# Kernel optimization log

Hardware: AMD Instinct MI355X
Metric: run time of the kernel (lower is better)

The kernel has to match this reference:

```python
import jax, jax.numpy as jnp
import numpy as np

B, C, NP, NT, D = 512, 3, 49, 76, 768
EPS = 0.1        # Sinkhorn entropic regularization
THRESH = 0.01    # convergence threshold on mean |r - r0|
MAX_ITER = 100


def _normalize(x, axis=-1):
    n = jnp.linalg.norm(x, axis=axis, keepdims=True)
    return x / jnp.maximum(n, 1e-12)


def _sinkhorn(K, u, v):
    # K: [B, n, m], u: [B, n], v: [B, m]. Faithful to the torch loop with
    # early exit: do-while via lax.while_loop (err check after each update).
    def cond(state):
        _, _, err, i = state
        return (i < MAX_ITER) & (err >= THRESH)

    def body(state):
        r, c, _, i = state
        r_new = u / jnp.einsum('bnm,bm->bn', K, c)
        c_new = v / jnp.einsum('bnm,bn->bm', K, r_new)
        err = jnp.mean(jnp.abs(r_new - r))
        return (r_new, c_new, err, i + 1)

    r0 = jnp.ones_like(u)
    c0 = jnp.ones_like(v)
    r, c, _, _ = jax.lax.while_loop(
        cond, body, (r0, c0, jnp.asarray(jnp.inf, K.dtype), 0))
    return r[..., :, None] * c[..., None, :] * K  # transport plan T


def _cross_entropy(logits):
    # labels = arange(B) (diagonal targets)
    logp = jax.nn.log_softmax(logits, axis=-1)
    return -jnp.mean(jnp.diagonal(logp))


def setup_inputs() -> dict:
    key = jax.random.key(0)
    k1, k2, k3, k4 = jax.random.split(key, 4)
    return {
        'image_features': jax.random.normal(k1, (B, C, D), jnp.float32),
        'text_features': jax.random.normal(k2, (B, C, D), jnp.float32),
        'logit_scale': jnp.full((1,), 100.0, jnp.float32),
        'local_image_features': jax.random.normal(k3, (B, C, NP, D), jnp.float32),
        'local_text_features': jax.random.normal(k4, (B, C, NT, D), jnp.float32),
    }


def reference(image_features, text_features, logit_scale,
              local_image_features, local_text_features):
    scale = logit_scale.reshape(())
    li = _normalize(local_image_features)          # [B, C, 49, D]
    lt = _normalize(local_text_features)           # [B, C, 76, D]
    # per-channel token similarity: [B, C, 49, 76]
    sim = jnp.einsum('bcnd,bcmd->bcnm', li, lt)
    # Sinkhorn is under no_grad in the original -> stop_gradient on K and T.
    K = jax.lax.stop_gradient(jnp.exp(-(1.0 - sim) / EPS))
    u = jnp.full((B, NP), 1.0 / NP, sim.dtype)
    v = jnp.full((B, NT), 1.0 / NT, sim.dtype)
    ot_loss = jnp.asarray(0.0, sim.dtype)
    for ch in range(C):  # per-channel Sinkhorn (independent early stopping)
        T = jax.lax.stop_gradient(_sinkhorn(K[:, ch], u, v))
        ot_loss = ot_loss + jnp.sum(T * sim[:, ch])
    # logits averaged over the 3 channels (sum over c folded into einsum)
    logits_per_image = scale * jnp.einsum(
        'bcd,ncd->bn', image_features, text_features) / C
    logits_per_text = logits_per_image.T
    total_loss = (_cross_entropy(logits_per_image)
                  + _cross_entropy(logits_per_text)) / 2 + ot_loss
    return total_loss
```

## Files before the change

### kernel.cpp

```cpp
#include <hip/hip_runtime.h>

#define NB 512
#define NC 3
#define NP_ 49
#define NT_ 76
#define DD 768

typedef __attribute__((ext_vector_type(8))) short bf16x8;
typedef __attribute__((ext_vector_type(4))) float f32x4;

__device__ inline unsigned short f2bf(float x) {
    unsigned int u = __float_as_uint(x);
    u += 0x7FFFu + ((u >> 16) & 1u);
    return (unsigned short)(u >> 16);
}
__device__ inline float bf_lo(unsigned int w) { return __uint_as_float(w << 16); }
__device__ inline float bf_hi(unsigned int w) { return __uint_as_float(w & 0xFFFF0000u); }

__global__ __launch_bounds__(256) void sink_kernel(const float* __restrict__ lif,
                                                   const float* __restrict__ ltf,
                                                   float* __restrict__ out) {
    const int tid = threadIdx.x;
    const int bc  = blockIdx.x;
    const float* ga = lif + (size_t)bc * (NP_ * DD);
    const float* gb = ltf + (size_t)bc * (NT_ * DD);

    __shared__ __attribute__((aligned(16))) unsigned short a_buf[64 * 72];
    __shared__ __attribute__((aligned(16))) unsigned short b_buf[80 * 72];
    __shared__ float Kmat[NP_ * 77];
    __shared__ float s_inv[144];
    __shared__ float r_vec[64];
    __shared__ float c_vec[80];
    __shared__ float s_err[4];
    __shared__ float s_red[4];

    for (int idx = tid; idx < 15 * 72; idx += 256) a_buf[49 * 72 + idx] = 0;
    for (int idx = tid; idx < 4 * 72;  idx += 256) b_buf[76 * 72 + idx] = 0;

    const int wave = tid >> 6;
    const int lane = tid & 63;
    const int lr = lane & 15;
    const int lk = lane >> 4;

    f32x4 acc[4][5];
    const f32x4 zero4 = {0.f, 0.f, 0.f, 0.f};
#pragma unroll
    for (int tn = 0; tn < 4; ++tn)
#pragma unroll
        for (int j = 0; j < 5; ++j) acc[tn][j] = zero4;

    float na = 0.f, nb = 0.f;

    for (int cc = 0; cc < 12; ++cc) {
        const int k0 = cc * 64;
        for (int idx = tid; idx < NP_ * 16; idx += 256) {
            int row = idx >> 4, q = idx & 15;
            const float4 v = *(const float4*)(ga + row * DD + k0 + q * 4);
            unsigned int w0 = (unsigned int)f2bf(v.x) | ((unsigned int)f2bf(v.y) << 16);
            unsigned int w1 = (unsigned int)f2bf(v.z) | ((unsigned int)f2bf(v.w) << 16);
            *(uint2*)(a_buf + row * 72 + q * 4) = make_uint2(w0, w1);
        }
        for (int idx = tid; idx < NT_ * 16; idx += 256) {
            int row = idx >> 4, q = idx & 15;
            const float4 v = *(const float4*)(gb + row * DD + k0 + q * 4);
            unsigned int w0 = (unsigned int)f2bf(v.x) | ((unsigned int)f2bf(v.y) << 16);
            unsigned int w1 = (unsigned int)f2bf(v.z) | ((unsigned int)f2bf(v.w) << 16);
            *(uint2*)(b_buf + row * 72 + q * 4) = make_uint2(w0, w1);
        }
        __syncthreads();
        if (wave == 0) {
#pragma unroll
            for (int ks = 0; ks < 2; ++ks) {
                bf16x8 bv[5];
#pragma unroll
                for (int j = 0; j < 5; ++j)
                    bv[j] = *(const bf16x8*)(b_buf + (j * 16 + lr) * 72 + ks * 32 + lk * 8);
#pragma unroll
                for (int tn = 0; tn < 4; ++tn) {
                    bf16x8 av = *(const bf16x8*)(a_buf + (tn * 16 + lr) * 72 + ks * 32 + lk * 8);
#pragma unroll
                    for (int j = 0; j < 5; ++j)
                        acc[tn][j] = __builtin_amdgcn_mfma_f32_16x16x32_bf16(av, bv[j], acc[tn][j], 0, 0, 0);
                }
            }
        } else if (wave == 1) {
            if (lane < NP_) {
                const unsigned int* ap = (const unsigned int*)(a_buf + lane * 72);
#pragma unroll
                for (int k = 0; k < 32; ++k) {
                    unsigned int w = ap[k];
                    float x = bf_lo(w), y = bf_hi(w);
                    na += x * x + y * y;
                }
            }
        } else {
            int j = tid - 128;
            if (j < NT_) {
                const unsigned int* bp = (const unsigned int*)(b_buf + j * 72);
#pragma unroll
                for (int k = 0; k < 32; ++k) {
                    unsigned int w = bp[k];
                    float x = bf_lo(w), y = bf_hi(w);
                    nb += x * x + y * y;
                }
            }
        }
        __syncthreads();
    }

    if (wave == 1 && lane < NP_) s_inv[lane] = 1.0f / fmaxf(sqrtf(na), 1e-12f);
    if (tid >= 128 && (tid - 128) < NT_) s_inv[64 + (tid - 128)] = 1.0f / fmaxf(sqrtf(nb), 1e-12f);
    __syncthreads();

    if (wave == 0) {
#pragma unroll
        for (int tn = 0; tn < 4; ++tn)
#pragma unroll
            for (int j = 0; j < 5; ++j)
#pragma unroll
                for (int rg = 0; rg < 4; ++rg) {
                    int n = tn * 16 + lk * 4 + rg;
                    int m = j * 16 + lr;
                    if (n < NP_ && m < NT_) {
                        float simv = acc[tn][j][rg] * s_inv[n] * s_inv[64 + m];
                        Kmat[n * 77 + m] = __expf((simv - 1.0f) * 10.0f);
                    }
                }
    }
    if (tid < NT_) c_vec[tid] = 1.0f;
    __syncthreads();

    const int n1 = tid >> 2, seg1 = tid & 3;
    const int n1c = (n1 < NP_) ? n1 : 0;
    float Kv1[19];
#pragma unroll
    for (int i = 0; i < 19; ++i)
        Kv1[i] = (tid < 196) ? Kmat[n1c * 77 + seg1 * 19 + i] : 0.0f;

    const int m2 = tid >> 1, seg2 = tid & 1;
    const int n2base = seg2 * 25;
    float Kv2[25];
#pragma unroll
    for (int i = 0; i < 25; ++i) {
        int nn = n2base + i;
        int nc = (nn < NP_) ? nn : 0;
        Kv2[i] = (tid < 152 && nn < NP_) ? Kmat[nc * 77 + m2] : 0.0f;
    }

    float r_old = 1.0f;
    float err;
    int iter = 0;
    do {
        float y = 0.f;
#pragma unroll
        for (int i = 0; i < 19; ++i) y += Kv1[i] * c_vec[seg1 * 19 + i];
        y += __shfl_xor(y, 1);
        y += __shfl_xor(y, 2);
        float rn = (1.0f / 49.0f) / y;
        float de = 0.f;
        if (tid < 196) {
            de = fabsf(rn - r_old);
            r_old = rn;
            if (seg1 == 0) r_vec[n1] = rn;
        }
        float e = de;
#pragma unroll
        for (int o = 1; o < 64; o <<= 1) e += __shfl_xor(e, o);
        if (lane == 0) s_err[wave] = e;
        __syncthreads();
        err = (s_err[0] + s_err[1] + s_err[2] + s_err[3]) * (1.0f / (4.0f * 49.0f));

        float z = 0.f;
#pragma unroll
        for (int i = 0; i < 25; ++i) {
            int nn = n2base + i;
            z += Kv2[i] * r_vec[(nn < NP_) ? nn : 0];
        }
        z += __shfl_xor(z, 1);
        if (tid < 152 && seg2 == 0) c_vec[m2] = (1.0f / 76.0f) / z;
        ++iter;
        __syncthreads();
    } while (iter < 100 && err >= 1e-3f);

    float part = 0.f;
    for (int e0 = tid; e0 < NP_ * NT_; e0 += 256) {
        int n = e0 / NT_;
        int m = e0 - n * NT_;
        float kv = Kmat[n * 77 + m];
        part += r_vec[n] * c_vec[m] * kv * (__logf(kv) * 0.1f + 1.0f);
    }
#pragma unroll
    for (int o = 1; o < 64; o <<= 1) part += __shfl_xor(part, o);
    if (lane == 0) s_red[wave] = part;
    __syncthreads();
    if (tid == 0) atomicAdd(out, s_red[0] + s_red[1] + s_red[2] + s_red[3]);
}

__global__ __launch_bounds__(256) void gemm_logits(const float* __restrict__ A,
                                                   const float* __restrict__ Bm,
                                                   float* __restrict__ L) {
    __shared__ __attribute__((aligned(16))) float At[64 * 36];
    __shared__ __attribute__((aligned(16))) float Bt[64 * 36];
    const int tid = threadIdx.x;
    const int i0 = blockIdx.x * 64, j0 = blockIdx.y * 64, kbase = blockIdx.z * 576;
    const int ty = tid >> 4, tx = tid & 15;
    float accv[4][4] = {};
    for (int kc = 0; kc < 18; ++kc) {
        int kb = kbase + kc * 32;
#pragma unroll
        for (int t = 0; t < 2; ++t) {
            int idx = tid + t * 256;
            int row = idx >> 3, q = idx & 7;
            *(float4*)(At + row * 36 + q * 4) =
                *(const float4*)(A + (size_t)(i0 + row) * 2304 + kb + q * 4);
            *(float4*)(Bt + row * 36 + q * 4) =
                *(const float4*)(Bm + (size_t)(j0 + row) * 2304 + kb + q * 4);
        }
        __syncthreads();
#pragma unroll 8
        for (int k = 0; k < 32; ++k) {
            float ra[4], rb[4];
#pragma unroll
            for (int a = 0; a < 4; ++a) ra[a] = At[(ty + 16 * a) * 36 + k];
#pragma unroll
            for (int b = 0; b < 4; ++b) rb[b] = Bt[(tx + 16 * b) * 36 + k];
#pragma unroll
            for (int a = 0; a < 4; ++a)
#pragma unroll
                for (int b = 0; b < 4; ++b) accv[a][b] += ra[a] * rb[b];
        }
        __syncthreads();
    }
#pragma unroll
    for (int a = 0; a < 4; ++a)
#pragma unroll
        for (int b = 0; b < 4; ++b)
            atomicAdd(L + (size_t)(i0 + ty + 16 * a) * 512 + (j0 + tx + 16 * b), accv[a][b]);
}

__device__ inline float blk_max(float v, float* sred, int wave, int lane) {
#pragma unroll
    for (int o = 1; o < 64; o <<= 1) v = fmaxf(v, __shfl_xor(v, o));
    if (lane == 0) sred[wave] = v;
    __syncthreads();
    v = fmaxf(fmaxf(sred[0], sred[1]), fmaxf(sred[2], sred[3]));
    __syncthreads();
    return v;
}
__device__ inline float blk_sum(float v, float* sred, int wave, int lane) {
#pragma unroll
    for (int o = 1; o < 64; o <<= 1) v += __shfl_xor(v, o);
    if (lane == 0) sred[wave] = v;
    __syncthreads();
    v = sred[0] + sred[1] + sred[2] + sred[3];
    __syncthreads();
    return v;
}

__global__ __launch_bounds__(256) void ce_kernel(const float* __restrict__ L,
                                                 const float* __restrict__ lsc,
                                                 float* __restrict__ out) {
    __shared__ float sred[4];
    const int i = blockIdx.x, tid = threadIdx.x;
    const int wave = tid >> 6, lane = tid & 63;
    const float s = lsc[0] * (1.0f / 3.0f);

    float xr0 = L[(size_t)i * 512 + tid] * s;
    float xr1 = L[(size_t)i * 512 + tid + 256] * s;
    float xc0 = L[(size_t)tid * 512 + i] * s;
    float xc1 = L[(size_t)(tid + 256) * 512 + i] * s;

    float mr = blk_max(fmaxf(xr0, xr1), sred, wave, lane);
    float sr = blk_sum(__expf(xr0 - mr) + __expf(xr1 - mr), sred, wave, lane);
    float lse_r = mr + __logf(sr);

    float mc = blk_max(fmaxf(xc0, xc1), sred, wave, lane);
    float sc = blk_sum(__expf(xc0 - mc) + __expf(xc1 - mc), sred, wave, lane);
    float lse_c = mc + __logf(sc);

    if (tid == 0) {
        float dii = L[(size_t)i * 512 + i] * s;
        atomicAdd(out, (lse_r + lse_c - 2.0f * dii) * (1.0f / 1024.0f));
    }
}

extern "C" void kernel_launch(void* const* d_in, const int* in_sizes, int n_in,
                              void* d_out, int out_size, void* d_ws, size_t ws_size,
                              hipStream_t stream) {
    const float* img = (const float*)d_in[0];
    const float* txt = (const float*)d_in[1];
    const float* lsc = (const float*)d_in[2];
    const float* lif = (const float*)d_in[3];
    const float* ltf = (const float*)d_in[4];
    float* out = (float*)d_out;
    float* Lws = (float*)d_ws;

    hipMemsetAsync(out, 0, sizeof(float), stream);
    hipMemsetAsync(Lws, 0, 512 * 512 * sizeof(float), stream);

    hipLaunchKernelGGL(gemm_logits, dim3(8, 8, 4), dim3(256), 0, stream, img, txt, Lws);
    hipLaunchKernelGGL(sink_kernel, dim3(NB * NC), dim3(256), 0, stream, lif, ltf, out);
    hipLaunchKernelGGL(ce_kernel, dim3(512), dim3(256), 0, stream, Lws, lsc, out);
}
```

Measured before the change: 763.0 us.

## Run Sinkhorn per channel in a single wave with direct global MFMA loads

Rewrites the Sinkhorn kernel to use one 64-lane wave per (batch, channel) block. The wave loads fp32 features straight from global memory into MFMA fragments, fusing the bf16 conversion and the norm accumulation, so the LDS staging and the block barriers go away. The Sinkhorn iterations keep K rows and columns in registers and reduce with wave shuffles, with no __syncthreads. This carries heavy register pressure (Kr, Kc and Kc2 arrays) and loses inter-wave parallelism within a block. Separately, the logits GEMM's split-K factor is doubled from 4 to 8.

```diff
diff --git a/kernel.cpp b/kernel.cpp
--- a/kernel.cpp
+++ b/kernel.cpp
@@ -14,33 +14,52 @@
     u += 0x7FFFu + ((u >> 16) & 1u);
     return (unsigned short)(u >> 16);
 }
-__device__ inline float bf_lo(unsigned int w) { return __uint_as_float(w << 16); }
-__device__ inline float bf_hi(unsigned int w) { return __uint_as_float(w & 0xFFFF0000u); }
-
-__global__ __launch_bounds__(256) void sink_kernel(const float* __restrict__ lif,
-                                                   const float* __restrict__ ltf,
-                                                   float* __restrict__ out) {
-    const int tid = threadIdx.x;
-    const int bc  = blockIdx.x;
+__device__ inline float bfval(unsigned short s) {
+    return __uint_as_float((unsigned int)s << 16);
+}
+__device__ inline float f4get(const float4& v, int e) {
+    return e == 0 ? v.x : e == 1 ? v.y : e == 2 ? v.z : v.w;
+}
+
+__device__ inline bf16x8 pack8(const float4& lo, const float4& hi, float& nrm) {
+    bf16x8 r;
+    unsigned short s; float x;
+    s = f2bf(lo.x); x = bfval(s); nrm += x * x; r[0] = (short)s;
+    s = f2bf(lo.y); x = bfval(s); nrm += x * x; r[1] = (short)s;
+    s = f2bf(lo.z); x = bfval(s); nrm += x * x; r[2] = (short)s;
+    s = f2bf(lo.w); x = bfval(s); nrm += x * x; r[3] = (short)s;
+    s = f2bf(hi.x); x = bfval(s); nrm += x * x; r[4] = (short)s;
+    s = f2bf(hi.y); x = bfval(s); nrm += x * x; r[5] = (short)s;
+    s = f2bf(hi.z); x = bfval(s); nrm += x * x; r[6] = (short)s;
+    s = f2bf(hi.w); x = bfval(s); nrm += x * x; r[7] = (short)s;
+    return r;
+}
+
+__global__ __launch_bounds__(64, 2) void sink_kernel(const float* __restrict__ lif,
+                                                     const float* __restrict__ ltf,
+                                                     float* __restrict__ out) {
+    const int lane = threadIdx.x;
+    const int bc   = blockIdx.x;
+    const int lr = lane & 15, lk = lane >> 4;
     const float* ga = lif + (size_t)bc * (NP_ * DD);
     const float* gb = ltf + (size_t)bc * (NT_ * DD);
 
-    __shared__ __attribute__((aligned(16))) unsigned short a_buf[64 * 72];
-    __shared__ __attribute__((aligned(16))) unsigned short b_buf[80 * 72];
     __shared__ float Kmat[NP_ * 77];
-    __shared__ float s_inv[144];
-    __shared__ float r_vec[64];
-    __shared__ float c_vec[80];
-    __shared__ float s_err[4];
-    __shared__ float s_red[4];
-
-    for (int idx = tid; idx < 15 * 72; idx += 256) a_buf[49 * 72 + idx] = 0;
-    for (int idx = tid; idx < 4 * 72;  idx += 256) b_buf[76 * 72 + idx] = 0;
-
-    const int wave = tid >> 6;
-    const int lane = tid & 63;
-    const int lr = lane & 15;
-    const int lk = lane >> 4;
+    __shared__ __attribute__((aligned(16))) float c_vec[80];
+    __shared__ __attribute__((aligned(16))) float r_vec[64];
+
+    const float* pa[4];
+#pragma unroll
+    for (int tn = 0; tn < 4; ++tn) {
+        int row = tn * 16 + lr; if (row > NP_ - 1) row = NP_ - 1;
+        pa[tn] = ga + row * DD + lk * 8;
+    }
+    const float* pb[5];
+#pragma unroll
+    for (int j = 0; j < 5; ++j) {
+        int row = j * 16 + lr; if (row > NT_ - 1) row = NT_ - 1;
+        pb[j] = gb + row * DD + lk * 8;
+    }
 
     f32x4 acc[4][5];
     const f32x4 zero4 = {0.f, 0.f, 0.f, 0.f};
@@ -48,152 +67,151 @@
     for (int tn = 0; tn < 4; ++tn)
 #pragma unroll
         for (int j = 0; j < 5; ++j) acc[tn][j] = zero4;
-
-    float na = 0.f, nb = 0.f;
-
-    for (int cc = 0; cc < 12; ++cc) {
-        const int k0 = cc * 64;
-        for (int idx = tid; idx < NP_ * 16; idx += 256) {
-            int row = idx >> 4, q = idx & 15;
-            const float4 v = *(const float4*)(ga + row * DD + k0 + q * 4);
-            unsigned int w0 = (unsigned int)f2bf(v.x) | ((unsigned int)f2bf(v.y) << 16);
-            unsigned int w1 = (unsigned int)f2bf(v.z) | ((unsigned int)f2bf(v.w) << 16);
-            *(uint2*)(a_buf + row * 72 + q * 4) = make_uint2(w0, w1);
-        }
-        for (int idx = tid; idx < NT_ * 16; idx += 256) {
-            int row = idx >> 4, q = idx & 15;
-            const float4 v = *(const float4*)(gb + row * DD + k0 + q * 4);
-            unsigned int w0 = (unsigned int)f2bf(v.x) | ((unsigned int)f2bf(v.y) << 16);
-            unsigned int w1 = (unsigned int)f2bf(v.z) | ((unsigned int)f2bf(v.w) << 16);
-            *(uint2*)(b_buf + row * 72 + q * 4) = make_uint2(w0, w1);
-        }
-        __syncthreads();
-        if (wave == 0) {
-#pragma unroll
-            for (int ks = 0; ks < 2; ++ks) {
-                bf16x8 bv[5];
-#pragma unroll
-                for (int j = 0; j < 5; ++j)
-                    bv[j] = *(const bf16x8*)(b_buf + (j * 16 + lr) * 72 + ks * 32 + lk * 8);
-#pragma unroll
-                for (int tn = 0; tn < 4; ++tn) {
-                    bf16x8 av = *(const bf16x8*)(a_buf + (tn * 16 + lr) * 72 + ks * 32 + lk * 8);
-#pragma unroll
-                    for (int j = 0; j < 5; ++j)
-                        acc[tn][j] = __builtin_amdgcn_mfma_f32_16x16x32_bf16(av, bv[j], acc[tn][j], 0, 0, 0);
-                }
-            }
-        } else if (wave == 1) {
-            if (lane < NP_) {
-                const unsigned int* ap = (const unsigned int*)(a_buf + lane * 72);
-#pragma unroll
-                for (int k = 0; k < 32; ++k) {
-                    unsigned int w = ap[k];
-                    float x = bf_lo(w), y = bf_hi(w);
-                    na += x * x + y * y;
-                }
-            }
-        } else {
-            int j = tid - 128;
-            if (j < NT_) {
-                const unsigned int* bp = (const unsigned int*)(b_buf + j * 72);
-#pragma unroll
-                for (int k = 0; k < 32; ++k) {
-                    unsigned int w = bp[k];
-                    float x = bf_lo(w), y = bf_hi(w);
-                    nb += x * x + y * y;
-                }
-            }
-        }
-        __syncthreads();
-    }
-
-    if (wave == 1 && lane < NP_) s_inv[lane] = 1.0f / fmaxf(sqrtf(na), 1e-12f);
-    if (tid >= 128 && (tid - 128) < NT_) s_inv[64 + (tid - 128)] = 1.0f / fmaxf(sqrtf(nb), 1e-12f);
-    __syncthreads();
-
-    if (wave == 0) {
+    float na[4] = {0.f, 0.f, 0.f, 0.f};
+    float nb[5] = {0.f, 0.f, 0.f, 0.f, 0.f};
+
+#pragma unroll 1
+    for (int cc = 0; cc < 24; ++cc) {
+        const int off = cc * 32;
+        float4 a0[4], a1[4], b0[5], b1[5];
+#pragma unroll
+        for (int tn = 0; tn < 4; ++tn) {
+            a0[tn] = *(const float4*)(pa[tn] + off);
+            a1[tn] = *(const float4*)(pa[tn] + off + 4);
+        }
+#pragma unroll
+        for (int j = 0; j < 5; ++j) {
+            b0[j] = *(const float4*)(pb[j] + off);
+            b1[j] = *(const float4*)(pb[j] + off + 4);
+        }
+        bf16x8 af[4], bfr[5];
+#pragma unroll
+        for (int tn = 0; tn < 4; ++tn) af[tn] = pack8(a0[tn], a1[tn], na[tn]);
+#pragma unroll
+        for (int j = 0; j < 5; ++j)  bfr[j] = pack8(b0[j], b1[j], nb[j]);
 #pragma unroll
         for (int tn = 0; tn < 4; ++tn)
 #pragma unroll
             for (int j = 0; j < 5; ++j)
-#pragma unroll
-                for (int rg = 0; rg < 4; ++rg) {
-                    int n = tn * 16 + lk * 4 + rg;
-                    int m = j * 16 + lr;
-                    if (n < NP_ && m < NT_) {
-                        float simv = acc[tn][j][rg] * s_inv[n] * s_inv[64 + m];
+                acc[tn][j] = __builtin_amdgcn_mfma_f32_16x16x32_bf16(af[tn], bfr[j], acc[tn][j], 0, 0, 0);
+    }
+
+#pragma unroll
+    for (int tn = 0; tn < 4; ++tn) {
+        float v = na[tn];
+        v += __shfl_xor(v, 16);
+        v += __shfl_xor(v, 32);
+        na[tn] = 1.0f / fmaxf(sqrtf(v), 1e-12f);
+    }
+#pragma unroll
+    for (int j = 0; j < 5; ++j) {
+        float v = nb[j];
+        v += __shfl_xor(v, 16);
+        v += __shfl_xor(v, 32);
+        nb[j] = 1.0f / fmaxf(sqrtf(v), 1e-12f);
+    }
+
+#pragma unroll
+    for (int tn = 0; tn < 4; ++tn)
+#pragma unroll
+        for (int rg = 0; rg < 4; ++rg) {
+            const int n = tn * 16 + lk * 4 + rg;
+            const float ia = __shfl(na[tn], lk * 4 + rg);
+            if (n < NP_) {
+#pragma unroll
+                for (int j = 0; j < 5; ++j) {
+                    const int m = j * 16 + lr;
+                    if (m < NT_) {
+                        const float simv = acc[tn][j][rg] * ia * nb[j];
                         Kmat[n * 77 + m] = __expf((simv - 1.0f) * 10.0f);
                     }
                 }
-    }
-    if (tid < NT_) c_vec[tid] = 1.0f;
-    __syncthreads();
-
-    const int n1 = tid >> 2, seg1 = tid & 3;
-    const int n1c = (n1 < NP_) ? n1 : 0;
-    float Kv1[19];
-#pragma unroll
-    for (int i = 0; i < 19; ++i)
-        Kv1[i] = (tid < 196) ? Kmat[n1c * 77 + seg1 * 19 + i] : 0.0f;
-
-    const int m2 = tid >> 1, seg2 = tid & 1;
-    const int n2base = seg2 * 25;
-    float Kv2[25];
-#pragma unroll
-    for (int i = 0; i < 25; ++i) {
-        int nn = n2base + i;
-        int nc = (nn < NP_) ? nn : 0;
-        Kv2[i] = (tid < 152 && nn < NP_) ? Kmat[nc * 77 + m2] : 0.0f;
+            }
+        }
+
+    c_vec[lane] = 1.0f;
+    if (lane < 16) c_vec[64 + lane] = 1.0f;
+
+    const int nrow = (lane < NP_) ? lane : 0;
+    float Kr[NT_];
+#pragma unroll
+    for (int m = 0; m < NT_; ++m)
+        Kr[m] = (lane < NP_) ? Kmat[nrow * 77 + m] : 0.0f;
+
+    const int col2 = (lane < 12) ? (64 + lane) : (NT_ - 1);
+    float Kc[NP_], Kc2[NP_];
+#pragma unroll
+    for (int n = 0; n < NP_; ++n) {
+        Kc[n]  = Kmat[n * 77 + lane];
+        Kc2[n] = Kmat[n * 77 + col2];
     }
 
     float r_old = 1.0f;
     float err;
     int iter = 0;
     do {
-        float y = 0.f;
-#pragma unroll
-        for (int i = 0; i < 19; ++i) y += Kv1[i] * c_vec[seg1 * 19 + i];
-        y += __shfl_xor(y, 1);
-        y += __shfl_xor(y, 2);
-        float rn = (1.0f / 49.0f) / y;
-        float de = 0.f;
-        if (tid < 196) {
-            de = fabsf(rn - r_old);
-            r_old = rn;
-            if (seg1 == 0) r_vec[n1] = rn;
-        }
+        float y0 = 0.f, y1 = 0.f, y2 = 0.f, y3 = 0.f;
+#pragma unroll
+        for (int q = 0; q < 19; ++q) {
+            const float4 cq = *(const float4*)(c_vec + q * 4);
+#pragma unroll
+            for (int e = 0; e < 4; ++e) {
+                const int i = 4 * q + e;
+                const float cv = f4get(cq, e);
+                if (i < 19)      y0 += Kr[i] * cv;
+                else if (i < 38) y1 += Kr[i] * cv;
+                else if (i < 57) y2 += Kr[i] * cv;
+                else             y3 += Kr[i] * cv;
+            }
+        }
+        const float y  = (y0 + y1) + (y2 + y3);
+        const float rn = (1.0f / 49.0f) / y;
+        const float de = (lane < NP_) ? fabsf(rn - r_old) : 0.0f;
+        r_old = rn;
+        r_vec[lane] = rn;
+
         float e = de;
-#pragma unroll
-        for (int o = 1; o < 64; o <<= 1) e += __shfl_xor(e, o);
-        if (lane == 0) s_err[wave] = e;
-        __syncthreads();
-        err = (s_err[0] + s_err[1] + s_err[2] + s_err[3]) * (1.0f / (4.0f * 49.0f));
-
-        float z = 0.f;
-#pragma unroll
-        for (int i = 0; i < 25; ++i) {
-            int nn = n2base + i;
-            z += Kv2[i] * r_vec[(nn < NP_) ? nn : 0];
-        }
-        z += __shfl_xor(z, 1);
-        if (tid < 152 && seg2 == 0) c_vec[m2] = (1.0f / 76.0f) / z;
+        e += __shfl_xor(e, 1);
+        e += __shfl_xor(e, 2);
+        e += __shfl_xor(e, 4);
+        e += __shfl_xor(e, 8);
+        const float g0 = __shfl(e, 0),  g1 = __shfl(e, 16);
+        const float g2 = __shfl(e, 32), g3 = __shfl(e, 48);
+        err = (((g0 + g1) + g2) + g3) * (1.0f / 49.0f);
+
+        float z0 = 0.f, z1 = 0.f, w0 = 0.f, w1 = 0.f;
+#pragma unroll
+        for (int q = 0; q < 13; ++q) {
+            const float4 rq = *(const float4*)(r_vec + q * 4);
+#pragma unroll
+            for (int e2 = 0; e2 < 4; ++e2) {
+                const int n = 4 * q + e2;
+                const float rv = f4get(rq, e2);
+                if (n < 25)      { z0 += Kc[n] * rv; w0 += Kc2[n] * rv; }
+                else if (n < 49) { z1 += Kc[n] * rv; w1 += Kc2[n] * rv; }
+            }
+        }
+        c_vec[lane] = (1.0f / 76.0f) / (z0 + z1);
+        if (lane < 12) c_vec[64 + lane] = (1.0f / 76.0f) / (w0 + w1);
         ++iter;
-        __syncthreads();
     } while (iter < 100 && err >= 1e-3f);
 
     float part = 0.f;
-    for (int e0 = tid; e0 < NP_ * NT_; e0 += 256) {
-        int n = e0 / NT_;
-        int m = e0 - n * NT_;
-        float kv = Kmat[n * 77 + m];
-        part += r_vec[n] * c_vec[m] * kv * (__logf(kv) * 0.1f + 1.0f);
+    if (lane < NP_) {
+        const float rr = r_old;
+#pragma unroll
+        for (int q = 0; q < 19; ++q) {
+            const float4 cq = *(const float4*)(c_vec + q * 4);
+#pragma unroll
+            for (int e2 = 0; e2 < 4; ++e2) {
+                const float kv = Kr[4 * q + e2];
+                part += rr * f4get(cq, e2) * kv * (__logf(kv) * 0.1f + 1.0f);
+            }
+        }
     }
 #pragma unroll
     for (int o = 1; o < 64; o <<= 1) part += __shfl_xor(part, o);
-    if (lane == 0) s_red[wave] = part;
-    __syncthreads();
-    if (tid == 0) atomicAdd(out, s_red[0] + s_red[1] + s_red[2] + s_red[3]);
+    if (lane == 0) atomicAdd(out, part);
 }
 
 __global__ __launch_bounds__(256) void gemm_logits(const float* __restrict__ A,
@@ -202,10 +220,10 @@
     __shared__ __attribute__((aligned(16))) float At[64 * 36];
     __shared__ __attribute__((aligned(16))) float Bt[64 * 36];
     const int tid = threadIdx.x;
-    const int i0 = blockIdx.x * 64, j0 = blockIdx.y * 64, kbase = blockIdx.z * 576;
+    const int i0 = blockIdx.x * 64, j0 = blockIdx.y * 64, kbase = blockIdx.z * 288;
     const int ty = tid >> 4, tx = tid & 15;
     float accv[4][4] = {};
-    for (int kc = 0; kc < 18; ++kc) {
+    for (int kc = 0; kc < 9; ++kc) {
         int kb = kbase + kc * 32;
 #pragma unroll
         for (int t = 0; t < 2; ++t) {
@@ -298,7 +316,7 @@
     hipMemsetAsync(out, 0, sizeof(float), stream);
     hipMemsetAsync(Lws, 0, 512 * 512 * sizeof(float), stream);
 
-    hipLaunchKernelGGL(gemm_logits, dim3(8, 8, 4), dim3(256), 0, stream, img, txt, Lws);
-    hipLaunchKernelGGL(sink_kernel, dim3(NB * NC), dim3(256), 0, stream, lif, ltf, out);
+    hipLaunchKernelGGL(gemm_logits, dim3(8, 8, 8), dim3(256), 0, stream, img, txt, Lws);
+    hipLaunchKernelGGL(sink_kernel, dim3(NB * NC), dim3(64), 0, stream, lif, ltf, out);
     hipLaunchKernelGGL(ce_kernel, dim3(512), dim3(256), 0, stream, Lws, lsc, out);
 }
```

Measured after the change: 669.5 us. 1.14x faster.
